# Optimization experiments

Hardware: AMD Instinct MI355X
Metric: run time of the kernel (lower is better)

## Reference

```python
import jax, jax.numpy as jnp
import numpy as np

N, K, D = 524288, 32, 8
EPS = 1e-6


def setup_inputs() -> dict:
    key = jax.random.key(0)
    k1, k2, k3, k4 = jax.random.split(key, 4)
    x = jax.random.normal(k1, (N, D), dtype=jnp.float32)
    pi = jax.random.uniform(k2, (K,), dtype=jnp.float32)
    means = jax.random.normal(k3, (K, D), dtype=jnp.float32)
    # eye + small perturbation keeps tril(chol_var) well-conditioned (PD covariance)
    chol_var = jnp.eye(D, dtype=jnp.float32)[None] + 0.1 * jax.random.normal(k4, (K, D, D), dtype=jnp.float32)
    return {"x": x, "pi": pi, "means": means, "chol_var": chol_var}


def reference(x, pi, means, chol_var):
    d = x.shape[-1]
    L = jnp.tril(chol_var)                                   # [K,d,d]
    cov = jnp.einsum('kij,klj->kil', L, L) + EPS * jnp.eye(d, dtype=x.dtype)
    C = jnp.linalg.cholesky(cov)                             # [K,d,d] (MVN recomputes cholesky)
    logdet = 2.0 * jnp.sum(jnp.log(jnp.diagonal(C, axis1=-2, axis2=-1)), axis=-1)  # [K]
    eye = jnp.eye(d, dtype=x.dtype)
    Cinv = jax.vmap(lambda c: jax.scipy.linalg.solve_triangular(c, eye, lower=True))(C)  # [K,d,d]
    zx = jnp.einsum('kij,nj->nki', Cinv, x)                  # [N,K,d]
    zm = jnp.einsum('kij,kj->ki', Cinv, means)               # [K,d]
    maha = jnp.sum((zx - zm[None]) ** 2, axis=-1)            # [N,K]
    log_2pi = jnp.log(2.0 * jnp.pi).astype(x.dtype)
    log_probs = -0.5 * (maha + d * log_2pi + logdet[None])   # [N,K]
    wll = log_probs + jax.nn.log_softmax(pi)[None]
    return jax.scipy.special.logsumexp(wll, axis=1)          # [N]
```

## Files before the change

kernel.cpp:

```cpp
#include <hip/hip_runtime.h>
#include <math.h>

#define K_ 32
#define D_ 8
#define EPS_ 1e-6f
#define CSTRIDE 48

typedef __attribute__((ext_vector_type(16))) float f32x16;

__global__ void gmm_precompute(const float* __restrict__ pi,
                               const float* __restrict__ means,
                               const float* __restrict__ chol,
                               float* __restrict__ cv) {
    int k = threadIdx.x;
    if (k >= K_) return;

    float L[D_][D_];
#pragma unroll
    for (int i = 0; i < D_; ++i)
#pragma unroll
        for (int j = 0; j < D_; ++j)
            L[i][j] = (j <= i) ? chol[k * D_ * D_ + i * D_ + j] : 0.f;

    float cov[D_][D_];
#pragma unroll
    for (int i = 0; i < D_; ++i)
#pragma unroll
        for (int j = 0; j < D_; ++j) {
            float s = 0.f;
            if (j <= i) {
#pragma unroll
                for (int m = 0; m < D_; ++m) s += L[i][m] * L[j][m];
                if (i == j) s += EPS_;
            }
            cov[i][j] = s;
        }

    float C[D_][D_];
#pragma unroll
    for (int i = 0; i < D_; ++i)
#pragma unroll
        for (int j = 0; j < D_; ++j) C[i][j] = 0.f;
#pragma unroll
    for (int j = 0; j < D_; ++j) {
        float s = cov[j][j];
#pragma unroll
        for (int m = 0; m < D_; ++m)
            if (m < j) s -= C[j][m] * C[j][m];
        float cjj = sqrtf(s);
        C[j][j] = cjj;
        float inv = 1.f / cjj;
#pragma unroll
        for (int i = 0; i < D_; ++i)
            if (i > j) {
                float t = cov[i][j];
#pragma unroll
                for (int m = 0; m < D_; ++m)
                    if (m < j) t -= C[i][m] * C[j][m];
                C[i][j] = t * inv;
            }
    }

    float logdet = 0.f;
#pragma unroll
    for (int i = 0; i < D_; ++i) logdet += __logf(C[i][i]);
    logdet *= 2.f;

    float Ci[D_][D_];
#pragma unroll
    for (int i = 0; i < D_; ++i)
#pragma unroll
        for (int j = 0; j < D_; ++j) Ci[i][j] = 0.f;
#pragma unroll
    for (int j = 0; j < D_; ++j) {
        Ci[j][j] = 1.f / C[j][j];
#pragma unroll
        for (int i = 0; i < D_; ++i)
            if (i > j) {
                float s = 0.f;
#pragma unroll
                for (int m = 0; m < D_; ++m)
                    if (m >= j && m < i) s += C[i][m] * Ci[m][j];
                Ci[i][j] = -s / C[i][i];
            }
    }

    float zm[D_];
#pragma unroll
    for (int i = 0; i < D_; ++i) {
        float s = 0.f;
#pragma unroll
        for (int j = 0; j < D_; ++j)
            if (j <= i) s += Ci[i][j] * means[k * D_ + j];
        zm[i] = s;
    }

    float mx = pi[0];
#pragma unroll
    for (int t = 1; t < K_; ++t) mx = fmaxf(mx, pi[t]);
    float se = 0.f;
#pragma unroll
    for (int t = 0; t < K_; ++t) se += __expf(pi[t] - mx);
    float lse = mx + __logf(se);

    const float LOG2PI = 1.8378770664093453f;
    const float SQH = 0.70710678118654752f;
    float cst = (pi[k] - lse) - 0.5f * (logdet + (float)D_ * LOG2PI);

    float* p = cv + k * CSTRIDE;
    int t = 0;
#pragma unroll
    for (int i = 0; i < D_; ++i)
#pragma unroll
        for (int j = 0; j < D_; ++j)
            if (j <= i) p[t++] = Ci[i][j] * SQH;
#pragma unroll
    for (int i = 0; i < D_; ++i) p[36 + i] = zm[i] * SQH;
    p[44] = cst;
    p[45] = 0.f; p[46] = 0.f; p[47] = 0.f;
}

#define CC(j) ((j) < 16 ? c0[(j)] : ((j) < 32 ? c1[(j) - 16] : c2[(j) - 32]))

__global__ __launch_bounds__(256) void gmm_main(const float* __restrict__ x,
                                                const float* __restrict__ cv,
                                                float* __restrict__ out, int N) {
    const int half = N >> 1;
    const int t = blockIdx.x * 256 + threadIdx.x;
    if (t >= half) return;
    const int n0 = t;
    const int n1 = t + half;

    const float4* xp0 = (const float4*)x + (size_t)n0 * 2;
    const float4* xp1 = (const float4*)x + (size_t)n1 * 2;
    float4 a0 = xp0[0], b0 = xp0[1];
    float4 a1 = xp1[0], b1 = xp1[1];
    float x0[D_] = {a0.x, a0.y, a0.z, a0.w, b0.x, b0.y, b0.z, b0.w};
    float x1[D_] = {a1.x, a1.y, a1.z, a1.w, b1.x, b1.y, b1.z, b1.w};

    float m0 = -INFINITY, s0 = 0.f;
    float m1 = -INFINITY, s1 = 0.f;

#pragma unroll 1
    for (int k = 0; k < K_; ++k) {
        const unsigned long long p =
            (unsigned long long)(const void*)(cv + k * CSTRIDE);
        f32x16 c0, c1, c2;
        asm("s_load_dwordx16 %0, %3, 0x0\n\t"
            "s_load_dwordx16 %1, %3, 0x40\n\t"
            "s_load_dwordx16 %2, %3, 0x80\n\t"
            "s_waitcnt lgkmcnt(0)"
            : "=&s"(c0), "=&s"(c1), "=&s"(c2)
            : "s"(p));

        float w0 = CC(44);
        float w1 = CC(44);
        int tt = 0;
#pragma unroll
        for (int i = 0; i < D_; ++i) {
            float z0 = -CC(36 + i);
            float z1 = -CC(36 + i);
#pragma unroll
            for (int j = 0; j <= i; ++j) {
                z0 = fmaf(CC(tt + j), x0[j], z0);
                z1 = fmaf(CC(tt + j), x1[j], z1);
            }
            tt += i + 1;
            w0 = fmaf(-z0, z0, w0);
            w1 = fmaf(-z1, z1, w1);
        }

        {
            float d = w0 - m0;
            float e = __expf(-fabsf(d));
            s0 = (d > 0.f) ? fmaf(s0, e, 1.f) : (s0 + e);
            m0 = fmaxf(m0, w0);
        }
        {
            float d = w1 - m1;
            float e = __expf(-fabsf(d));
            s1 = (d > 0.f) ? fmaf(s1, e, 1.f) : (s1 + e);
            m1 = fmaxf(m1, w1);
        }
    }

    out[n0] = m0 + __logf(s0);
    out[n1] = m1 + __logf(s1);
}

extern "C" void kernel_launch(void* const* d_in, const int* in_sizes, int n_in,
                              void* d_out, int out_size, void* d_ws, size_t ws_size,
                              hipStream_t stream) {
    const float* x     = (const float*)d_in[0];
    const float* pi    = (const float*)d_in[1];
    const float* means = (const float*)d_in[2];
    const float* chol  = (const float*)d_in[3];
    float* out = (float*)d_out;
    float* cv  = (float*)d_ws;

    int N = in_sizes[0] / D_;

    gmm_precompute<<<1, 64, 0, stream>>>(pi, means, chol, cv);
    int half = N >> 1;
    gmm_main<<<(half + 255) / 256, 256, 0, stream>>>(x, cv, out, N);
}
```

Before: 91.89 us.

## Process four points per thread and skip cov/Cholesky recompute in precompute

After: 87.31 us. -5.0%, faster.

```diff
diff --git a/kernel.cpp b/kernel.cpp
--- a/kernel.cpp
+++ b/kernel.cpp
@@ -3,8 +3,8 @@
 
 #define K_ 32
 #define D_ 8
-#define EPS_ 1e-6f
 #define CSTRIDE 48
+#define S_ 4
 
 typedef __attribute__((ext_vector_type(16))) float f32x16;
 
@@ -19,79 +19,37 @@
 #pragma unroll
     for (int i = 0; i < D_; ++i)
 #pragma unroll
-        for (int j = 0; j < D_; ++j)
-            L[i][j] = (j <= i) ? chol[k * D_ * D_ + i * D_ + j] : 0.f;
+        for (int j = 0; j <= i; ++j)
+            L[i][j] = chol[k * D_ * D_ + i * D_ + j];
 
-    float cov[D_][D_];
+    float rd[D_];
 #pragma unroll
-    for (int i = 0; i < D_; ++i)
-#pragma unroll
-        for (int j = 0; j < D_; ++j) {
-            float s = 0.f;
-            if (j <= i) {
-#pragma unroll
-                for (int m = 0; m < D_; ++m) s += L[i][m] * L[j][m];
-                if (i == j) s += EPS_;
-            }
-            cov[i][j] = s;
-        }
+    for (int i = 0; i < D_; ++i) rd[i] = 1.f / L[i][i];
 
-    float C[D_][D_];
-#pragma unroll
-    for (int i = 0; i < D_; ++i)
-#pragma unroll
-        for (int j = 0; j < D_; ++j) C[i][j] = 0.f;
+    float Ci[D_][D_];
 #pragma unroll
     for (int j = 0; j < D_; ++j) {
-        float s = cov[j][j];
+        Ci[j][j] = rd[j];
 #pragma unroll
-        for (int m = 0; m < D_; ++m)
-            if (m < j) s -= C[j][m] * C[j][m];
-        float cjj = sqrtf(s);
-        C[j][j] = cjj;
-        float inv = 1.f / cjj;
+        for (int i = j + 1; i < D_; ++i) {
+            float s = 0.f;
 #pragma unroll
-        for (int i = 0; i < D_; ++i)
-            if (i > j) {
-                float t = cov[i][j];
-#pragma unroll
-                for (int m = 0; m < D_; ++m)
-                    if (m < j) t -= C[i][m] * C[j][m];
-                C[i][j] = t * inv;
-            }
+            for (int m = j; m < i; ++m) s += L[i][m] * Ci[m][j];
+            Ci[i][j] = -s * rd[i];
+        }
     }
 
     float logdet = 0.f;
 #pragma unroll
-    for (int i = 0; i < D_; ++i) logdet += __logf(C[i][i]);
+    for (int i = 0; i < D_; ++i) logdet += __logf(fabsf(L[i][i]));
     logdet *= 2.f;
-
-    float Ci[D_][D_];
-#pragma unroll
-    for (int i = 0; i < D_; ++i)
-#pragma unroll
-        for (int j = 0; j < D_; ++j) Ci[i][j] = 0.f;
-#pragma unroll
-    for (int j = 0; j < D_; ++j) {
-        Ci[j][j] = 1.f / C[j][j];
-#pragma unroll
-        for (int i = 0; i < D_; ++i)
-            if (i > j) {
-                float s = 0.f;
-#pragma unroll
-                for (int m = 0; m < D_; ++m)
-                    if (m >= j && m < i) s += C[i][m] * Ci[m][j];
-                Ci[i][j] = -s / C[i][i];
-            }
-    }
 
     float zm[D_];
 #pragma unroll
     for (int i = 0; i < D_; ++i) {
         float s = 0.f;
 #pragma unroll
-        for (int j = 0; j < D_; ++j)
-            if (j <= i) s += Ci[i][j] * means[k * D_ + j];
+        for (int j = 0; j <= i; ++j) s += Ci[i][j] * means[k * D_ + j];
         zm[i] = s;
     }
 
@@ -112,8 +70,7 @@
 #pragma unroll
     for (int i = 0; i < D_; ++i)
 #pragma unroll
-        for (int j = 0; j < D_; ++j)
-            if (j <= i) p[t++] = Ci[i][j] * SQH;
+        for (int j = 0; j <= i; ++j) p[t++] = Ci[i][j] * SQH;
 #pragma unroll
     for (int i = 0; i < D_; ++i) p[36 + i] = zm[i] * SQH;
     p[44] = cst;
@@ -125,21 +82,22 @@
 __global__ __launch_bounds__(256) void gmm_main(const float* __restrict__ x,
                                                 const float* __restrict__ cv,
                                                 float* __restrict__ out, int N) {
-    const int half = N >> 1;
+    const int q = N >> 2;
     const int t = blockIdx.x * 256 + threadIdx.x;
-    if (t >= half) return;
-    const int n0 = t;
-    const int n1 = t + half;
+    if (t >= q) return;
 
-    const float4* xp0 = (const float4*)x + (size_t)n0 * 2;
-    const float4* xp1 = (const float4*)x + (size_t)n1 * 2;
-    float4 a0 = xp0[0], b0 = xp0[1];
-    float4 a1 = xp1[0], b1 = xp1[1];
-    float x0[D_] = {a0.x, a0.y, a0.z, a0.w, b0.x, b0.y, b0.z, b0.w};
-    float x1[D_] = {a1.x, a1.y, a1.z, a1.w, b1.x, b1.y, b1.z, b1.w};
+    float xv[S_][D_];
+#pragma unroll
+    for (int s = 0; s < S_; ++s) {
+        const float4* xp = (const float4*)x + (size_t)(t + s * q) * 2;
+        float4 a = xp[0], b = xp[1];
+        xv[s][0] = a.x; xv[s][1] = a.y; xv[s][2] = a.z; xv[s][3] = a.w;
+        xv[s][4] = b.x; xv[s][5] = b.y; xv[s][6] = b.z; xv[s][7] = b.w;
+    }
 
-    float m0 = -INFINITY, s0 = 0.f;
-    float m1 = -INFINITY, s1 = 0.f;
+    float m[S_], sm[S_];
+#pragma unroll
+    for (int s = 0; s < S_; ++s) { m[s] = -INFINITY; sm[s] = 0.f; }
 
 #pragma unroll 1
     for (int k = 0; k < K_; ++k) {
@@ -153,39 +111,37 @@
             : "=&s"(c0), "=&s"(c1), "=&s"(c2)
             : "s"(p));
 
-        float w0 = CC(44);
-        float w1 = CC(44);
+        float w[S_];
+#pragma unroll
+        for (int s = 0; s < S_; ++s) w[s] = CC(44);
         int tt = 0;
 #pragma unroll
         for (int i = 0; i < D_; ++i) {
-            float z0 = -CC(36 + i);
-            float z1 = -CC(36 + i);
+            float z[S_];
 #pragma unroll
-            for (int j = 0; j <= i; ++j) {
-                z0 = fmaf(CC(tt + j), x0[j], z0);
-                z1 = fmaf(CC(tt + j), x1[j], z1);
-            }
+            for (int s = 0; s < S_; ++s) z[s] = -CC(36 + i);
+#pragma unroll
+            for (int j = 0; j <= i; ++j)
+#pragma unroll
+                for (int s = 0; s < S_; ++s)
+                    z[s] = fmaf(CC(tt + j), xv[s][j], z[s]);
             tt += i + 1;
-            w0 = fmaf(-z0, z0, w0);
-            w1 = fmaf(-z1, z1, w1);
+#pragma unroll
+            for (int s = 0; s < S_; ++s) w[s] = fmaf(-z[s], z[s], w[s]);
         }
 
-        {
-            float d = w0 - m0;
+#pragma unroll
+        for (int s = 0; s < S_; ++s) {
+            float d = w[s] - m[s];
             float e = __expf(-fabsf(d));
-            s0 = (d > 0.f) ? fmaf(s0, e, 1.f) : (s0 + e);
-            m0 = fmaxf(m0, w0);
-        }
-        {
-            float d = w1 - m1;
-            float e = __expf(-fabsf(d));
-            s1 = (d > 0.f) ? fmaf(s1, e, 1.f) : (s1 + e);
-            m1 = fmaxf(m1, w1);
+            sm[s] = (d > 0.f) ? fmaf(sm[s], e, 1.f) : (sm[s] + e);
+            m[s] = fmaxf(m[s], w[s]);
         }
     }
 
-    out[n0] = m0 + __logf(s0);
-    out[n1] = m1 + __logf(s1);
+#pragma unroll
+    for (int s = 0; s < S_; ++s)
+        out[t + s * q] = m[s] + __logf(sm[s]);
 }
 
 extern "C" void kernel_launch(void* const* d_in, const int* in_sizes, int n_in,
@@ -201,6 +157,6 @@
     int N = in_sizes[0] / D_;
 
     gmm_precompute<<<1, 64, 0, stream>>>(pi, means, chol, cv);
-    int half = N >> 1;
-    gmm_main<<<(half + 255) / 256, 256, 0, stream>>>(x, cv, out, N);
+    int q = N >> 2;
+    gmm_main<<<(q + 255) / 256, 256, 0, stream>>>(x, cv, out, N);
 }
```
